# Kernel tuning notes

Measured on AMD Instinct MI355X. Metric: run time of the kernel, lower is better.

The kernel has to match this reference:

```python
import jax, jax.numpy as jnp
import numpy as np

D_MODEL = 256
N_HEADS = 8
N_LEVELS = 3
N_POINTS = 4
HEAD_DIM = D_MODEL // N_HEADS
SPATIAL_SHAPES = [(80, 80), (40, 40), (20, 20)]
B = 16
LEN_Q = 300
N_TOTAL = sum(h * w for h, w in SPATIAL_SHAPES)  # 8400
N_LP = N_LEVELS * N_POINTS


def setup_inputs() -> dict:
    key = jax.random.key(0)
    ks = jax.random.split(key, 8)
    s = 0.02
    return {
        "query": jax.random.normal(ks[0], (B, LEN_Q, D_MODEL), jnp.float32),
        "reference_points": jax.random.uniform(ks[1], (B, LEN_Q, N_LEVELS, 2), jnp.float32),
        "input_flatten": jax.random.normal(ks[2], (B, N_TOTAL, D_MODEL), jnp.float32),
        "W_off": jax.random.normal(ks[3], (D_MODEL, N_HEADS * N_LP * 2), jnp.float32) * s,
        "b_off": jnp.zeros((N_HEADS * N_LP * 2,), jnp.float32),
        "W_attn": jax.random.normal(ks[4], (D_MODEL, N_HEADS * N_LP), jnp.float32) * s,
        "b_attn": jnp.zeros((N_HEADS * N_LP,), jnp.float32),
        "W_val": jax.random.normal(ks[5], (D_MODEL, D_MODEL), jnp.float32) * s,
        "b_val": jnp.zeros((D_MODEL,), jnp.float32),
        "W_out": jax.random.normal(ks[6], (D_MODEL, D_MODEL), jnp.float32) * s,
        "b_out": jnp.zeros((D_MODEL,), jnp.float32),
    }


def _ms_deform_core(value, sampling_locations, attention_weights):
    # value: (B, n_heads, head_dim, N_total); locations: (B, Lq, H, L, P, 2) in [0,1]
    Bq, Lq = sampling_locations.shape[0], sampling_locations.shape[1]
    BN = Bq * N_HEADS
    grids = 2.0 * sampling_locations - 1.0
    starts = np.cumsum([0] + [h * w for h, w in SPATIAL_SHAPES])
    sampled_levels = []
    for lid, (H, W) in enumerate(SPATIAL_SHAPES):
        val_l = value[..., starts[lid]:starts[lid + 1]]                    # (B,H,hd,HW)
        val_flat = val_l.reshape(BN, HEAD_DIM, H * W).transpose(0, 2, 1)   # (BN,HW,hd)
        g = grids[:, :, :, lid].transpose(0, 2, 1, 3, 4).reshape(BN, Lq, N_POINTS, 2)
        ix = ((g[..., 0] + 1.0) * W - 1.0) / 2.0
        iy = ((g[..., 1] + 1.0) * H - 1.0) / 2.0
        ix0 = jnp.floor(ix).astype(jnp.int32)
        iy0 = jnp.floor(iy).astype(jnp.int32)
        ix1 = ix0 + 1
        iy1 = iy0 + 1
        fx = (ix - ix0.astype(ix.dtype))[..., None]
        fy = (iy - iy0.astype(iy.dtype))[..., None]

        def corner(iyc, ixc):
            valid = ((ixc >= 0) & (ixc < W) & (iyc >= 0) & (iyc < H)).astype(val_flat.dtype)
            idx = (jnp.clip(iyc, 0, H - 1) * W + jnp.clip(ixc, 0, W - 1))
            idx = idx.reshape(BN, Lq * N_POINTS, 1)
            v = jnp.take_along_axis(val_flat, idx, axis=1)
            return v.reshape(BN, Lq, N_POINTS, HEAD_DIM) * valid[..., None]

        v00 = corner(iy0, ix0)
        v01 = corner(iy0, ix1)
        v10 = corner(iy1, ix0)
        v11 = corner(iy1, ix1)
        sampled = ((1 - fx) * (1 - fy)) * v00 + (fx * (1 - fy)) * v01 \
                + ((1 - fx) * fy) * v10 + (fx * fy) * v11
        sampled_levels.append(sampled.transpose(0, 3, 1, 2))               # (BN,hd,Lq,P)
    sv = jnp.stack(sampled_levels, axis=-2).reshape(BN, HEAD_DIM, Lq, N_LP)
    a = attention_weights.transpose(0, 2, 1, 3).reshape(BN, 1, Lq, N_LP)
    out = jnp.sum(sv * a, axis=-1)                                         # (BN,hd,Lq)
    return out.reshape(Bq, D_MODEL, Lq).transpose(0, 2, 1)                 # (B,Lq,D)


def reference(query, reference_points, input_flatten,
              W_off, b_off, W_attn, b_attn, W_val, b_val, W_out, b_out):
    Bq, Lq = query.shape[0], query.shape[1]
    value = input_flatten @ W_val + b_val
    value = value.reshape(Bq, -1, N_HEADS, HEAD_DIM).transpose(0, 2, 3, 1)  # (B,H,hd,N)
    off = (query @ W_off + b_off).reshape(Bq, Lq, N_HEADS, N_LEVELS, N_POINTS, 2)
    attn = jax.nn.softmax((query @ W_attn + b_attn).reshape(Bq, Lq, N_HEADS, N_LP), axis=-1)
    # offset normalizer is (W,H) per level (x first)
    norm = jnp.array([[w, h] for h, w in SPATIAL_SHAPES], jnp.float32)
    loc = reference_points[:, :, None, :, None, :] + off / norm[None, None, None, :, None, :]
    out = _ms_deform_core(value, loc, attn)
    return out @ W_out + b_out
```

## Files before the change

### kernel.cpp

```cpp
#include <hip/hip_runtime.h>
#include <hip/hip_bf16.h>

#define DM 256
#define NH 8
#define HD 32
#define NLV 3
#define NPT 4
#define NLP 12
#define BB 16
#define LQ 300
#define NT 8400
#define MROWS (BB * NT)
#define QROWS (BB * LQ)
#define KP3 264
#define VB (MROWS / 64)

typedef __bf16 bf16x8 __attribute__((ext_vector_type(8)));
typedef float  f32x16 __attribute__((ext_vector_type(16)));

__global__ void k_wt(const float* __restrict__ W_val,
                     const float* __restrict__ W_off,
                     const float* __restrict__ W_attn,
                     const float* __restrict__ W_out,
                     __hip_bfloat16* __restrict__ Wf,
                     __hip_bfloat16* __restrict__ Wf2,
                     __hip_bfloat16* __restrict__ Wf3)
{
    const int n = blockIdx.x;
    const int k = threadIdx.x;
    if (n < 256) {
        Wf[(size_t)(k >> 3) * 2048 + n * 8 + (k & 7)] =
            __float2bfloat16(W_val[(size_t)k * 256 + n]);
    } else if (n < 544) {
        const int n2 = n - 256;
        float v = (n2 < 192) ? W_off[(size_t)k * 192 + n2]
                             : W_attn[(size_t)k * 96 + (n2 - 192)];
        Wf2[(size_t)(k >> 3) * 2304 + n2 * 8 + (k & 7)] = __float2bfloat16(v);
    } else {
        const int n3 = n - 544;
        Wf3[(size_t)(k >> 3) * 2048 + n3 * 8 + (k & 7)] =
            __float2bfloat16(W_out[(size_t)k * 256 + n3]);
    }
}

__global__ __launch_bounds__(256) void k_mm1(
    const float* __restrict__ A,
    const __hip_bfloat16* __restrict__ Wf,
    const float* __restrict__ bval,
    __hip_bfloat16* __restrict__ V,
    const float* __restrict__ Q,
    const __hip_bfloat16* __restrict__ Wf2,
    const float* __restrict__ boff,
    const float* __restrict__ battn,
    float* __restrict__ off_out,
    float* __restrict__ attn_out)
{
    __shared__ __hip_bfloat16 As[64 * KP3];

    const int t    = threadIdx.x;
    const int wave = t >> 6;
    const int lane = t & 63;
    const int lm   = lane & 31;
    const int kh   = lane >> 5;
    const int lk   = kh * 8;

    if (blockIdx.x < VB) {
        const int m0  = blockIdx.x * 64;
        const int ar2 = t >> 2;
        const int ak2 = (t & 3) * 16;

        const float* ap = A + (size_t)(m0 + ar2) * 256 + ak2;
        float4 r[16];
#pragma unroll
        for (int it = 0; it < 4; ++it)
#pragma unroll
            for (int c = 0; c < 4; ++c)
                r[it * 4 + c] = *(const float4*)(ap + it * 64 + c * 4);

#pragma unroll
        for (int it = 0; it < 4; ++it) {
            union { __hip_bfloat162 h2[4]; bf16x8 v; } u0, u1;
            u0.h2[0] = __float22bfloat162_rn(make_float2(r[it*4+0].x, r[it*4+0].y));
            u0.h2[1] = __float22bfloat162_rn(make_float2(r[it*4+0].z, r[it*4+0].w));
            u0.h2[2] = __float22bfloat162_rn(make_float2(r[it*4+1].x, r[it*4+1].y));
            u0.h2[3] = __float22bfloat162_rn(make_float2(r[it*4+1].z, r[it*4+1].w));
            u1.h2[0] = __float22bfloat162_rn(make_float2(r[it*4+2].x, r[it*4+2].y));
            u1.h2[1] = __float22bfloat162_rn(make_float2(r[it*4+2].z, r[it*4+2].w));
            u1.h2[2] = __float22bfloat162_rn(make_float2(r[it*4+3].x, r[it*4+3].y));
            u1.h2[3] = __float22bfloat162_rn(make_float2(r[it*4+3].z, r[it*4+3].w));
            *(bf16x8*)(&As[ar2 * KP3 + it * 64 + ak2])     = u0.v;
            *(bf16x8*)(&As[ar2 * KP3 + it * 64 + ak2 + 8]) = u1.v;
        }
        __syncthreads();

        f32x16 acc[2][2];
#pragma unroll
        for (int i = 0; i < 2; i++)
#pragma unroll
            for (int j = 0; j < 2; j++)
#pragma unroll
                for (int e = 0; e < 16; e++) acc[i][j][e] = 0.f;

        const __hip_bfloat16* wf0 = Wf + (size_t)(wave * 64 + lm) * 8 + kh * 2048;

#pragma unroll
        for (int ks = 0; ks < 16; ++ks) {
            bf16x8 af0 = *(const bf16x8*)(&As[(lm)      * KP3 + ks * 16 + lk]);
            bf16x8 af1 = *(const bf16x8*)(&As[(32 + lm) * KP3 + ks * 16 + lk]);
            bf16x8 b0  = *(const bf16x8*)(wf0 + (size_t)ks * 4096);
            bf16x8 b1  = *(const bf16x8*)(wf0 + (size_t)ks * 4096 + 256);
            acc[0][0] = __builtin_amdgcn_mfma_f32_32x32x16_bf16(af0, b0, acc[0][0], 0, 0, 0);
            acc[0][1] = __builtin_amdgcn_mfma_f32_32x32x16_bf16(af0, b1, acc[0][1], 0, 0, 0);
            acc[1][0] = __builtin_amdgcn_mfma_f32_32x32x16_bf16(af1, b0, acc[1][0], 0, 0, 0);
            acc[1][1] = __builtin_amdgcn_mfma_f32_32x32x16_bf16(af1, b1, acc[1][1], 0, 0, 0);
        }

        const int bb  = m0 / NT;
        const int bnd = (bb + 1) * NT;
#pragma unroll
        for (int i = 0; i < 2; i++) {
#pragma unroll
            for (int j = 0; j < 2; j++) {
                const int n  = wave * 64 + j * 32 + lm;
                const float bn = bval[n];
                const int h  = n >> 5;
                const int d  = n & 31;
#pragma unroll
                for (int r2 = 0; r2 < 16; r2++) {
                    int rl = (r2 & 3) + 8 * (r2 >> 2) + 4 * kh;
                    int m  = m0 + i * 32 + rl;
                    int b  = bb + ((m >= bnd) ? 1 : 0);
                    int pos = m - b * NT;
                    V[((size_t)(b * NH + h) * NT + pos) * HD + d] =
                        __float2bfloat16(acc[i][j][r2] + bn);
                }
            }
        }
    } else {
        const int m0 = (blockIdx.x - VB) * 32;
        const int ar = t >> 3;
        const int ak = (t & 7) * 8;

        const float* ap = Q + (size_t)(m0 + ar) * 256 + ak;
        float4 r[8];
#pragma unroll
        for (int it = 0; it < 4; ++it) {
            r[it * 2 + 0] = *(const float4*)(ap + it * 64);
            r[it * 2 + 1] = *(const float4*)(ap + it * 64 + 4);
        }
#pragma unroll
        for (int it = 0; it < 4; ++it) {
            union { __hip_bfloat162 h2[4]; bf16x8 v; } ua;
            ua.h2[0] = __float22bfloat162_rn(make_float2(r[it*2+0].x, r[it*2+0].y));
            ua.h2[1] = __float22bfloat162_rn(make_float2(r[it*2+0].z, r[it*2+0].w));
            ua.h2[2] = __float22bfloat162_rn(make_float2(r[it*2+1].x, r[it*2+1].y));
            ua.h2[3] = __float22bfloat162_rn(make_float2(r[it*2+1].z, r[it*2+1].w));
            *(bf16x8*)(&As[ar * KP3 + it * 64 + ak]) = ua.v;
        }
        __syncthreads();

        f32x16 acc[3];
#pragma unroll
        for (int j = 0; j < 3; j++)
#pragma unroll
            for (int e = 0; e < 16; e++) acc[j][e] = 0.f;

        const __hip_bfloat16* wf0 = Wf2 + (size_t)(wave * 96 + lm) * 8 + kh * 2304;

        if (wave < 3) {
#pragma unroll
            for (int ks = 0; ks < 16; ++ks) {
                bf16x8 af = *(const bf16x8*)(&As[lm * KP3 + ks * 16 + lk]);
#pragma unroll
                for (int j = 0; j < 3; j++) {
                    bf16x8 bf = *(const bf16x8*)(wf0 + (size_t)ks * 4608 + j * 256);
                    acc[j] = __builtin_amdgcn_mfma_f32_32x32x16_bf16(af, bf, acc[j], 0, 0, 0);
                }
            }
#pragma unroll
            for (int j = 0; j < 3; j++) {
                const int n = wave * 96 + j * 32 + lm;
                const float bias_ = (n < 192) ? boff[n] : battn[n - 192];
#pragma unroll
                for (int r2 = 0; r2 < 16; r2++) {
                    int rl = (r2 & 3) + 8 * (r2 >> 2) + 4 * kh;
                    int m  = m0 + rl;
                    float v = acc[j][r2] + bias_;
                    if (n < 192) off_out[(size_t)m * 192 + n] = v;
                    else         attn_out[(size_t)m * 96 + (n - 192)] = v;
                }
            }
        }
    }
}

__global__ __launch_bounds__(256) void k_sample(
    const float* __restrict__ off_raw,
    const float* __restrict__ attn_raw,
    const float* __restrict__ refp,
    const __hip_bfloat16* __restrict__ V,
    __hip_bfloat16* __restrict__ sampled)
{
    const int t = threadIdx.x;

    const int bid  = blockIdx.x;
    const int xcd  = bid & 7;
    const int slot = bid >> 3;
    const int hi   = (slot >= 75) ? 1 : 0;
    const int b    = xcd + (hi << 3);
    const int q0   = (slot - hi * 75) * 4;
    const int bq0  = b * LQ + q0;

    __shared__ float aw[4][96];
    __shared__ float wc[4][96][4];
    __shared__ int   ic[4][96][4];

    if (t < 32) {
        const int q = t >> 3, h = t & 7;
        const float* arp = attn_raw + (size_t)(bq0 + q) * 96 + h * 12;
        float4 x0 = *(const float4*)arp;
        float4 x1 = *(const float4*)(arp + 4);
        float4 x2 = *(const float4*)(arp + 8);
        float v[12] = {x0.x, x0.y, x0.z, x0.w,
                       x1.x, x1.y, x1.z, x1.w,
                       x2.x, x2.y, x2.z, x2.w};
        float mx = -1e30f;
#pragma unroll
        for (int i = 0; i < 12; i++) mx = fmaxf(mx, v[i]);
        float s = 0.f;
#pragma unroll
        for (int i = 0; i < 12; i++) { v[i] = expf(v[i] - mx); s += v[i]; }
        float inv = 1.f / s;
#pragma unroll
        for (int i = 0; i < 12; i++) aw[q][h * 12 + i] = v[i] * inv;
    }
    __syncthreads();

#pragma unroll
    for (int i = t; i < 384; i += 256) {
        const int q  = i / 96;
        const int s  = i - q * 96;
        const int bq = bq0 + q;
        const float dims[3]  = {80.f, 40.f, 20.f};
        const int startsl[3] = {0, 6400, 8000};
        const int idiml[3]   = {80, 40, 20};
        int h = s / 12, lp = s - h * 12, l = lp >> 2, p = lp & 3;
        float2 o2 = *(const float2*)(off_raw + (size_t)bq * 192 + ((h * 3 + l) * 4 + p) * 2);
        float2 r2 = *(const float2*)(refp + (size_t)bq * 6 + l * 2);
        float D  = dims[l];
        float ix = (r2.x + o2.x / D) * D - 0.5f;
        float iy = (r2.y + o2.y / D) * D - 0.5f;
        const int Dl = idiml[l];
        const int st = startsl[l];

        float fix = floorf(ix), fiy = floorf(iy);
        int ix0 = (int)fix, iy0 = (int)fiy;
        int ix1 = ix0 + 1, iy1 = iy0 + 1;
        float fx = ix - fix, fy = iy - fiy;

        float mx0 = (ix0 >= 0 && ix0 < Dl) ? 1.f : 0.f;
        float mx1 = (ix1 >= 0 && ix1 < Dl) ? 1.f : 0.f;
        float my0 = (iy0 >= 0 && iy0 < Dl) ? 1.f : 0.f;
        float my1 = (iy1 >= 0 && iy1 < Dl) ? 1.f : 0.f;

        int cx0 = min(max(ix0, 0), Dl - 1);
        int cx1 = min(max(ix1, 0), Dl - 1);
        int cy0 = min(max(iy0, 0), Dl - 1);
        int cy1 = min(max(iy1, 0), Dl - 1);

        float a = aw[q][s];
        wc[q][s][0] = (1.f - fx) * (1.f - fy) * mx0 * my0 * a;
        wc[q][s][1] = fx * (1.f - fy) * mx1 * my0 * a;
        wc[q][s][2] = (1.f - fx) * fy * mx0 * my1 * a;
        wc[q][s][3] = fx * fy * mx1 * my1 * a;
        ic[q][s][0] = (st + cy0 * Dl + cx0) * HD;
        ic[q][s][1] = (st + cy0 * Dl + cx1) * HD;
        ic[q][s][2] = (st + cy1 * Dl + cx0) * HD;
        ic[q][s][3] = (st + cy1 * Dl + cx1) * HD;
    }
    __syncthreads();

    const int q  = t >> 6;
    const int u  = t & 63;
    const int h  = u >> 3;
    const int dt = (u & 7) * 4;
    const int bq = bq0 + q;
    const __hip_bfloat16* vb = V + (size_t)(b * NH + h) * NT * HD + dt;

    float a0 = 0.f, a1 = 0.f, a2 = 0.f, a3 = 0.f;
#pragma unroll
    for (int lp = 0; lp < 12; lp++) {
        const int s = h * 12 + lp;
        float4 w4 = *(const float4*)(&wc[q][s][0]);
        int4   i4 = *(const int4*)(&ic[q][s][0]);
        union { uint2 u2; __hip_bfloat162 h2[2]; } c0, c1, c2, c3;
        c0.u2 = *(const uint2*)(vb + i4.x);
        c1.u2 = *(const uint2*)(vb + i4.y);
        c2.u2 = *(const uint2*)(vb + i4.z);
        c3.u2 = *(const uint2*)(vb + i4.w);
        float2 f0a = __bfloat1622float2(c0.h2[0]), f0b = __bfloat1622float2(c0.h2[1]);
        float2 f1a = __bfloat1622float2(c1.h2[0]), f1b = __bfloat1622float2(c1.h2[1]);
        float2 f2a = __bfloat1622float2(c2.h2[0]), f2b = __bfloat1622float2(c2.h2[1]);
        float2 f3a = __bfloat1622float2(c3.h2[0]), f3b = __bfloat1622float2(c3.h2[1]);
        a0 = fmaf(w4.x, f0a.x, fmaf(w4.y, f1a.x, fmaf(w4.z, f2a.x, fmaf(w4.w, f3a.x, a0))));
        a1 = fmaf(w4.x, f0a.y, fmaf(w4.y, f1a.y, fmaf(w4.z, f2a.y, fmaf(w4.w, f3a.y, a1))));
        a2 = fmaf(w4.x, f0b.x, fmaf(w4.y, f1b.x, fmaf(w4.z, f2b.x, fmaf(w4.w, f3b.x, a2))));
        a3 = fmaf(w4.x, f0b.y, fmaf(w4.y, f1b.y, fmaf(w4.z, f2b.y, fmaf(w4.w, f3b.y, a3))));
    }
    union { ushort4 s4; __hip_bfloat162 h2[2]; } ou;
    ou.h2[0] = __float22bfloat162_rn(make_float2(a0, a1));
    ou.h2[1] = __float22bfloat162_rn(make_float2(a2, a3));
    *(ushort4*)(sampled + (size_t)bq * 256 + h * 32 + dt) = ou.s4;
}

__global__ __launch_bounds__(256) void k_outproj(
    const __hip_bfloat16* __restrict__ A,
    const __hip_bfloat16* __restrict__ Wf3,
    const float* __restrict__ bias,
    float* __restrict__ out)
{
    __shared__ __hip_bfloat16 As[32 * KP3];

    const int t    = threadIdx.x;
    const int m0   = blockIdx.x * 32;
    const int wave = t >> 6;
    const int lane = t & 63;
    const int lm   = lane & 31;
    const int kh   = lane >> 5;
    const int lk   = kh * 8;
    const int ar   = t >> 3;
    const int ak   = (t & 7) * 8;

    const __hip_bfloat16* apg = A + (size_t)(m0 + ar) * 256 + ak;
    bf16x8 rr[4];
#pragma unroll
    for (int it = 0; it < 4; ++it)
        rr[it] = *(const bf16x8*)(apg + it * 64);
#pragma unroll
    for (int it = 0; it < 4; ++it)
        *(bf16x8*)(&As[ar * KP3 + it * 64 + ak]) = rr[it];
    __syncthreads();

    f32x16 acc[2];
#pragma unroll
    for (int j = 0; j < 2; j++)
#pragma unroll
        for (int e = 0; e < 16; e++) acc[j][e] = 0.f;

    const __hip_bfloat16* wf0 = Wf3 + (size_t)(wave * 64 + lm) * 8 + kh * 2048;

#pragma unroll
    for (int ks = 0; ks < 16; ++ks) {
        bf16x8 af = *(const bf16x8*)(&As[lm * KP3 + ks * 16 + lk]);
        bf16x8 b0 = *(const bf16x8*)(wf0 + (size_t)ks * 4096);
        bf16x8 b1 = *(const bf16x8*)(wf0 + (size_t)ks * 4096 + 256);
        acc[0] = __builtin_amdgcn_mfma_f32_32x32x16_bf16(af, b0, acc[0], 0, 0, 0);
        acc[1] = __builtin_amdgcn_mfma_f32_32x32x16_bf16(af, b1, acc[1], 0, 0, 0);
    }

#pragma unroll
    for (int j = 0; j < 2; j++) {
        const int n = wave * 64 + j * 32 + lm;
        const float bn = bias[n];
#pragma unroll
        for (int r2 = 0; r2 < 16; r2++) {
            int rl = (r2 & 3) + 8 * (r2 >> 2) + 4 * kh;
            int m  = m0 + rl;
            out[(size_t)m * 256 + n] = acc[j][r2] + bn;
        }
    }
}

extern "C" void kernel_launch(void* const* d_in, const int* in_sizes, int n_in,
                              void* d_out, int out_size, void* d_ws, size_t ws_size,
                              hipStream_t stream) {
    const float* query  = (const float*)d_in[0];
    const float* refp   = (const float*)d_in[1];
    const float* inputf = (const float*)d_in[2];
    const float* W_off  = (const float*)d_in[3];
    const float* b_off  = (const float*)d_in[4];
    const float* W_attn = (const float*)d_in[5];
    const float* b_attn = (const float*)d_in[6];
    const float* W_val  = (const float*)d_in[7];
    const float* b_val  = (const float*)d_in[8];
    const float* W_out  = (const float*)d_in[9];
    const float* b_out  = (const float*)d_in[10];
    float* out = (float*)d_out;

    char* ws = (char*)d_ws;
    __hip_bfloat16* value   = (__hip_bfloat16*)ws;
    float* off_raw          = (float*)(ws + 68812800);
    float* attn_raw         = (float*)(ws + 72499200);
    __hip_bfloat16* sampled = (__hip_bfloat16*)(ws + 74342400);
    __hip_bfloat16* Wf      = (__hip_bfloat16*)(ws + 76800000);
    __hip_bfloat16* Wf2     = (__hip_bfloat16*)(ws + 76931072);
    __hip_bfloat16* Wf3     = (__hip_bfloat16*)(ws + 77078528);

    k_wt<<<800, 256, 0, stream>>>(W_val, W_off, W_attn, W_out, Wf, Wf2, Wf3);
    k_mm1<<<VB + QROWS / 32, 256, 0, stream>>>(
        inputf, Wf, b_val, value, query, Wf2, b_off, b_attn, off_raw, attn_raw);
    k_sample<<<1200, 256, 0, stream>>>(off_raw, attn_raw, refp, value, sampled);
    k_outproj<<<QROWS / 32, 256, 0, stream>>>(sampled, Wf3, b_out, out);
}
```

Measured before the change: 264.9 us.

## Stream GEMM A tiles via async global-to-LDS loads with double buffering

Rewrites the A-operand staging in the value and query projection GEMMs. Instead of loading the whole fp32 row tile into registers, converting it to bf16 and storing it to LDS, each block now issues global_load_lds DMA copies of fp32 K-chunks into a double-buffered, XOR-swizzled LDS buffer. The bf16 conversion happens when fragments are read from LDS, so the next chunk's load overlaps the current chunk's MFMAs. The cost is a doubled LDS footprint in fp32 (32 KB), extra barriers per K step, and repeated conversion work in every wave.

```diff
diff --git a/kernel.cpp b/kernel.cpp
--- a/kernel.cpp
+++ b/kernel.cpp
@@ -17,6 +17,9 @@
 
 typedef __bf16 bf16x8 __attribute__((ext_vector_type(8)));
 typedef float  f32x16 __attribute__((ext_vector_type(16)));
+
+#define GPTR(x) ((const __attribute__((address_space(1))) unsigned int*)(x))
+#define LPTR(x) ((__attribute__((address_space(3))) unsigned int*)(x))
 
 __global__ void k_wt(const float* __restrict__ W_val,
                      const float* __restrict__ W_off,
@@ -55,64 +58,77 @@
     float* __restrict__ off_out,
     float* __restrict__ attn_out)
 {
-    __shared__ __hip_bfloat16 As[64 * KP3];
+    __shared__ __align__(16) float Asf[8192];
 
     const int t    = threadIdx.x;
     const int wave = t >> 6;
     const int lane = t & 63;
     const int lm   = lane & 31;
     const int kh   = lane >> 5;
-    const int lk   = kh * 8;
 
     if (blockIdx.x < VB) {
-        const int m0  = blockIdx.x * 64;
-        const int ar2 = t >> 2;
-        const int ak2 = (t & 3) * 16;
-
-        const float* ap = A + (size_t)(m0 + ar2) * 256 + ak2;
-        float4 r[16];
-#pragma unroll
-        for (int it = 0; it < 4; ++it)
-#pragma unroll
-            for (int c = 0; c < 4; ++c)
-                r[it * 4 + c] = *(const float4*)(ap + it * 64 + c * 4);
+        const int m0 = blockIdx.x * 64;
+
+        f32x16 acc[2][2];
+#pragma unroll
+        for (int i = 0; i < 2; i++)
+#pragma unroll
+            for (int j = 0; j < 2; j++)
+#pragma unroll
+                for (int e = 0; e < 16; e++) acc[i][j][e] = 0.f;
+
+        const __hip_bfloat16* wf0 = Wf + (size_t)(wave * 64 + lm) * 8 + kh * 2048;
+        const int sw = lm & 15;
+
+#pragma unroll
+        for (int p = 0; p < 4; ++p) {
+            const int row = p * 16 + (t >> 4);
+            const int sc  = (t & 15) ^ (row & 15);
+            const float* gsrc = A + (size_t)(m0 + row) * 256 + sc * 4;
+            __builtin_amdgcn_global_load_lds(GPTR(gsrc),
+                LPTR((char*)Asf + p * 4096 + (t & 192) * 16), 16, 0, 0);
+        }
+        __syncthreads();
 
 #pragma unroll
         for (int it = 0; it < 4; ++it) {
-            union { __hip_bfloat162 h2[4]; bf16x8 v; } u0, u1;
-            u0.h2[0] = __float22bfloat162_rn(make_float2(r[it*4+0].x, r[it*4+0].y));
-            u0.h2[1] = __float22bfloat162_rn(make_float2(r[it*4+0].z, r[it*4+0].w));
-            u0.h2[2] = __float22bfloat162_rn(make_float2(r[it*4+1].x, r[it*4+1].y));
-            u0.h2[3] = __float22bfloat162_rn(make_float2(r[it*4+1].z, r[it*4+1].w));
-            u1.h2[0] = __float22bfloat162_rn(make_float2(r[it*4+2].x, r[it*4+2].y));
-            u1.h2[1] = __float22bfloat162_rn(make_float2(r[it*4+2].z, r[it*4+2].w));
-            u1.h2[2] = __float22bfloat162_rn(make_float2(r[it*4+3].x, r[it*4+3].y));
-            u1.h2[3] = __float22bfloat162_rn(make_float2(r[it*4+3].z, r[it*4+3].w));
-            *(bf16x8*)(&As[ar2 * KP3 + it * 64 + ak2])     = u0.v;
-            *(bf16x8*)(&As[ar2 * KP3 + it * 64 + ak2 + 8]) = u1.v;
-        }
-        __syncthreads();
-
-        f32x16 acc[2][2];
-#pragma unroll
-        for (int i = 0; i < 2; i++)
-#pragma unroll
-            for (int j = 0; j < 2; j++)
-#pragma unroll
-                for (int e = 0; e < 16; e++) acc[i][j][e] = 0.f;
-
-        const __hip_bfloat16* wf0 = Wf + (size_t)(wave * 64 + lm) * 8 + kh * 2048;
-
-#pragma unroll
-        for (int ks = 0; ks < 16; ++ks) {
-            bf16x8 af0 = *(const bf16x8*)(&As[(lm)      * KP3 + ks * 16 + lk]);
-            bf16x8 af1 = *(const bf16x8*)(&As[(32 + lm) * KP3 + ks * 16 + lk]);
-            bf16x8 b0  = *(const bf16x8*)(wf0 + (size_t)ks * 4096);
-            bf16x8 b1  = *(const bf16x8*)(wf0 + (size_t)ks * 4096 + 256);
-            acc[0][0] = __builtin_amdgcn_mfma_f32_32x32x16_bf16(af0, b0, acc[0][0], 0, 0, 0);
-            acc[0][1] = __builtin_amdgcn_mfma_f32_32x32x16_bf16(af0, b1, acc[0][1], 0, 0, 0);
-            acc[1][0] = __builtin_amdgcn_mfma_f32_32x32x16_bf16(af1, b0, acc[1][0], 0, 0, 0);
-            acc[1][1] = __builtin_amdgcn_mfma_f32_32x32x16_bf16(af1, b1, acc[1][1], 0, 0, 0);
+            float* cur = Asf + (it & 1) * 4096;
+            if (it < 3) {
+                float* nxt = Asf + ((it & 1) ^ 1) * 4096;
+#pragma unroll
+                for (int p = 0; p < 4; ++p) {
+                    const int row = p * 16 + (t >> 4);
+                    const int sc  = (t & 15) ^ (row & 15);
+                    const float* gsrc = A + (size_t)(m0 + row) * 256 + (it + 1) * 64 + sc * 4;
+                    __builtin_amdgcn_global_load_lds(GPTR(gsrc),
+                        LPTR((char*)nxt + p * 4096 + (t & 192) * 16), 16, 0, 0);
+                }
+            }
+#pragma unroll
+            for (int g4 = 0; g4 < 4; ++g4) {
+                const int g  = it * 4 + g4;
+                const int s0 = g4 * 4 + kh * 2;
+                float4 x0 = *(const float4*)(cur + lm * 64 + (((s0)     ^ sw) << 2));
+                float4 x1 = *(const float4*)(cur + lm * 64 + (((s0 + 1) ^ sw) << 2));
+                float4 y0 = *(const float4*)(cur + (32 + lm) * 64 + (((s0)     ^ sw) << 2));
+                float4 y1 = *(const float4*)(cur + (32 + lm) * 64 + (((s0 + 1) ^ sw) << 2));
+                union { __hip_bfloat162 h2[4]; bf16x8 v; } u0, u1;
+                u0.h2[0] = __float22bfloat162_rn(make_float2(x0.x, x0.y));
+                u0.h2[1] = __float22bfloat162_rn(make_float2(x0.z, x0.w));
+                u0.h2[2] = __float22bfloat162_rn(make_float2(x1.x, x1.y));
+                u0.h2[3] = __float22bfloat162_rn(make_float2(x1.z, x1.w));
+                u1.h2[0] = __float22bfloat162_rn(make_float2(y0.x, y0.y));
+                u1.h2[1] = __float22bfloat162_rn(make_float2(y0.z, y0.w));
+                u1.h2[2] = __float22bfloat162_rn(make_float2(y1.x, y1.y));
+                u1.h2[3] = __float22bfloat162_rn(make_float2(y1.z, y1.w));
+                bf16x8 b0 = *(const bf16x8*)(wf0 + (size_t)g * 4096);
+                bf16x8 b1 = *(const bf16x8*)(wf0 + (size_t)g * 4096 + 256);
+                acc[0][0] = __builtin_amdgcn_mfma_f32_32x32x16_bf16(u0.v, b0, acc[0][0], 0, 0, 0);
+                acc[0][1] = __builtin_amdgcn_mfma_f32_32x32x16_bf16(u0.v, b1, acc[0][1], 0, 0, 0);
+                acc[1][0] = __builtin_amdgcn_mfma_f32_32x32x16_bf16(u1.v, b0, acc[1][0], 0, 0, 0);
+                acc[1][1] = __builtin_amdgcn_mfma_f32_32x32x16_bf16(u1.v, b1, acc[1][1], 0, 0, 0);
+            }
+            if (it < 3) __syncthreads();
         }
 
         const int bb  = m0 / NT;
@@ -138,45 +154,63 @@
         }
     } else {
         const int m0 = (blockIdx.x - VB) * 32;
-        const int ar = t >> 3;
-        const int ak = (t & 7) * 8;
-
-        const float* ap = Q + (size_t)(m0 + ar) * 256 + ak;
-        float4 r[8];
+
+        f32x16 acc[3];
+#pragma unroll
+        for (int j = 0; j < 3; j++)
+#pragma unroll
+            for (int e = 0; e < 16; e++) acc[j][e] = 0.f;
+
+        const __hip_bfloat16* wf0 = Wf2 + (size_t)(wave * 96 + lm) * 8 + kh * 2304;
+        const int sw = lm & 15;
+
+#pragma unroll
+        for (int p = 0; p < 2; ++p) {
+            const int row = p * 16 + (t >> 4);
+            const int sc  = (t & 15) ^ (row & 15);
+            const float* gsrc = Q + (size_t)(m0 + row) * 256 + sc * 4;
+            __builtin_amdgcn_global_load_lds(GPTR(gsrc),
+                LPTR((char*)Asf + p * 4096 + (t & 192) * 16), 16, 0, 0);
+        }
+        __syncthreads();
+
 #pragma unroll
         for (int it = 0; it < 4; ++it) {
-            r[it * 2 + 0] = *(const float4*)(ap + it * 64);
-            r[it * 2 + 1] = *(const float4*)(ap + it * 64 + 4);
-        }
-#pragma unroll
-        for (int it = 0; it < 4; ++it) {
-            union { __hip_bfloat162 h2[4]; bf16x8 v; } ua;
-            ua.h2[0] = __float22bfloat162_rn(make_float2(r[it*2+0].x, r[it*2+0].y));
-            ua.h2[1] = __float22bfloat162_rn(make_float2(r[it*2+0].z, r[it*2+0].w));
-            ua.h2[2] = __float22bfloat162_rn(make_float2(r[it*2+1].x, r[it*2+1].y));
-            ua.h2[3] = __float22bfloat162_rn(make_float2(r[it*2+1].z, r[it*2+1].w));
-            *(bf16x8*)(&As[ar * KP3 + it * 64 + ak]) = ua.v;
-        }
-        __syncthreads();
-
-        f32x16 acc[3];
-#pragma unroll
-        for (int j = 0; j < 3; j++)
-#pragma unroll
-            for (int e = 0; e < 16; e++) acc[j][e] = 0.f;
-
-        const __hip_bfloat16* wf0 = Wf2 + (size_t)(wave * 96 + lm) * 8 + kh * 2304;
+            float* cur = Asf + (it & 1) * 2048;
+            if (it < 3) {
+                float* nxt = Asf + ((it & 1) ^ 1) * 2048;
+#pragma unroll
+                for (int p = 0; p < 2; ++p) {
+                    const int row = p * 16 + (t >> 4);
+                    const int sc  = (t & 15) ^ (row & 15);
+                    const float* gsrc = Q + (size_t)(m0 + row) * 256 + (it + 1) * 64 + sc * 4;
+                    __builtin_amdgcn_global_load_lds(GPTR(gsrc),
+                        LPTR((char*)nxt + p * 4096 + (t & 192) * 16), 16, 0, 0);
+                }
+            }
+            if (wave < 3) {
+#pragma unroll
+                for (int g4 = 0; g4 < 4; ++g4) {
+                    const int g  = it * 4 + g4;
+                    const int s0 = g4 * 4 + kh * 2;
+                    float4 x0 = *(const float4*)(cur + lm * 64 + (((s0)     ^ sw) << 2));
+                    float4 x1 = *(const float4*)(cur + lm * 64 + (((s0 + 1) ^ sw) << 2));
+                    union { __hip_bfloat162 h2[4]; bf16x8 v; } ua;
+                    ua.h2[0] = __float22bfloat162_rn(make_float2(x0.x, x0.y));
+                    ua.h2[1] = __float22bfloat162_rn(make_float2(x0.z, x0.w));
+                    ua.h2[2] = __float22bfloat162_rn(make_float2(x1.x, x1.y));
+                    ua.h2[3] = __float22bfloat162_rn(make_float2(x1.z, x1.w));
+#pragma unroll
+                    for (int j = 0; j < 3; j++) {
+                        bf16x8 bf = *(const bf16x8*)(wf0 + (size_t)g * 4608 + j * 256);
+                        acc[j] = __builtin_amdgcn_mfma_f32_32x32x16_bf16(ua.v, bf, acc[j], 0, 0, 0);
+                    }
+                }
+            }
+            if (it < 3) __syncthreads();
+        }
 
         if (wave < 3) {
-#pragma unroll
-            for (int ks = 0; ks < 16; ++ks) {
-                bf16x8 af = *(const bf16x8*)(&As[lm * KP3 + ks * 16 + lk]);
-#pragma unroll
-                for (int j = 0; j < 3; j++) {
-                    bf16x8 bf = *(const bf16x8*)(wf0 + (size_t)ks * 4608 + j * 256);
-                    acc[j] = __builtin_amdgcn_mfma_f32_32x32x16_bf16(af, bf, acc[j], 0, 0, 0);
-                }
-            }
 #pragma unroll
             for (int j = 0; j < 3; j++) {
                 const int n = wave * 96 + j * 32 + lm;
```

Result: no change. 262.3 us (-1.0%).
